# Optimization experiments

Measured on AMD Instinct MI355X. Metric: run time of the kernel, lower is better.

Reference implementation:

```python
import jax, jax.numpy as jnp
import numpy as np
from jax import lax

THRESHOLD = 0.25
DECAY = 0.9
STRIDE = 1
PADDING = 1


def setup_inputs() -> dict:
    key = jax.random.key(0)
    k1, k2 = jax.random.split(key)
    # binary spike train: (B, C_in, H, W, T)
    x = (jax.random.uniform(k1, (8, 16, 64, 64, 32)) < 0.2).astype(jnp.float32)
    # conv weight: (C_out, C_in, k, k), init ~ randn * 0.1 as in the torch module
    weight = jax.random.normal(k2, (32, 16, 3, 3), dtype=jnp.float32) * 0.1
    return {"x": x, "weight": weight}


def _conv(xt, weight):
    # xt: (B, C_in, H, W) -> (B, C_out, H_out, W_out)
    return lax.conv_general_dilated(
        xt, weight,
        window_strides=(STRIDE, STRIDE),
        padding=[(PADDING, PADDING), (PADDING, PADDING)],
        dimension_numbers=("NCHW", "OIHW", "NCHW"),
    )


def reference(x, weight):
    B, Cin, H, W, T = x.shape
    Cout, k = weight.shape[0], weight.shape[2]
    Hout = (H + 2 * PADDING - k) // STRIDE + 1
    Wout = (W + 2 * PADDING - k) // STRIDE + 1

    xt = jnp.moveaxis(x, -1, 0)  # (T, B, Cin, H, W)
    mem0 = jnp.zeros((B, Cout, Hout, Wout), dtype=jnp.float32)

    def step(mem, x_t):
        # accumulate conv activation, then decay (order matches original: += then *=)
        mem = (mem + _conv(x_t, weight)) * DECAY
        spike = (mem >= THRESHOLD).astype(mem.dtype)
        mem = mem * (1.0 - spike)  # reset fired neurons to 0
        return mem, spike

    _, spikes = lax.scan(step, mem0, xt)  # spikes: (T, B, Cout, Hout, Wout)
    return jnp.moveaxis(spikes, 0, -1)    # (B, Cout, Hout, Wout, T)
```

## Files before the change

kernel.cpp:

```cpp
#include <hip/hip_runtime.h>


#define BB   8
#define CIN  16
#define HH   64
#define WW   64
#define TT   32
#define COUT 32
#define HWT  (HH * WW * TT)

__global__ void repack_w(const float* __restrict__ wgt, float* __restrict__ wT) {
    const int e = blockIdx.x * 256 + threadIdx.x;
    if (e < 144 * 32) {
        const int co  = e & 31;
        const int tau = e >> 5;
        const int ci  = tau & 15;
        const int khw = tau >> 4;
        wT[tau * 32 + co] = wgt[co * 144 + ci * 9 + khw];
    }
}

__global__ __launch_bounds__(256)
void snn_main(const float* __restrict__ x, const float* __restrict__ wT,
              float* __restrict__ out) {
    const int tid  = threadIdx.x;
    const int lane = tid & 63;
    const int t    = lane & 31;
    const int wi   = (tid >> 5);
    const int w0   = blockIdx.x * 8;
    const int h    = blockIdx.y;
    const int b    = blockIdx.z;
    const int w    = w0 + wi;

    float acc[COUT];
#pragma unroll
    for (int c = 0; c < COUT; ++c) acc[c] = 0.0f;

#pragma unroll
    for (int kh = 0; kh < 3; ++kh) {
        const int hs = h + kh - 1;
        if ((unsigned)hs >= HH) continue;
#pragma unroll
        for (int kw = 0; kw < 3; ++kw) {
            const int ws    = w + kw - 1;
            const bool ok   = (unsigned)ws < WW;
            const int  wsc  = ok ? ws : 0;
            const float* xp = x + ((b * CIN * HH + hs) * WW + wsc) * TT + t;
#pragma unroll
            for (int ci = 0; ci < CIN; ++ci) {
                float xv = xp[ci * HWT];
                xv = ok ? xv : 0.0f;
                const float* wr = wT + ((kh * 3 + kw) * 16 + ci) * 32;
#pragma unroll
                for (int c = 0; c < COUT; ++c)
                    acc[c] = fmaf(xv, wr[c], acc[c]);
            }
        }
    }

    __shared__ float s_tr[256 * 36];
#pragma unroll
    for (int c = 0; c < COUT; ++c)
        s_tr[(c * 8 + wi) * 36 + t] = acc[c];
    __syncthreads();

    const int co2 = tid >> 3;
    const int wi2 = tid & 7;
    const float* rr = s_tr + (co2 * 8 + wi2) * 36;

    float* op = out + (((b * COUT + co2) * HH + h) * WW + (w0 + wi2)) * TT;
    float mem = 0.0f;
#pragma unroll
    for (int t4 = 0; t4 < TT; t4 += 4) {
        const float4 q = *reinterpret_cast<const float4*>(rr + t4);
        const float cv[4] = {q.x, q.y, q.z, q.w};
        float4 o;
        float* vp = &o.x;
#pragma unroll
        for (int j = 0; j < 4; ++j) {
            mem = (mem + cv[j]) * 0.9f;
            const bool sp = (mem >= 0.25f);
            vp[j] = sp ? 1.0f : 0.0f;
            if (sp) mem = 0.0f;
        }
        *reinterpret_cast<float4*>(op + t4) = o;
    }
}

extern "C" void kernel_launch(void* const* d_in, const int* in_sizes, int n_in,
                              void* d_out, int out_size, void* d_ws, size_t ws_size,
                              hipStream_t stream) {
    const float* x   = (const float*)d_in[0];
    const float* wgt = (const float*)d_in[1];
    float* out = (float*)d_out;
    float* wT  = (float*)d_ws;

    repack_w<<<18, 256, 0, stream>>>(wgt, wT);

    dim3 grid(WW / 8, HH, BB);
    snn_main<<<grid, dim3(256), 0, stream>>>(x, wT, out);
}
```

Measured before the change: 281.2 us.

## Use packed FP32 FMA, halve LDS transpose buffer, raise occupancy bound

Accumulators become 2-wide float vectors so the compiler can emit packed FP32 FMAs (v_pk_fma_f32) and take weights as 64-bit pairs. The shared-memory transpose buffer is halved and the scan runs in two passes over 16 channels each, so LDS per block drops. The launch bound requests 8 blocks per CU. The trade-offs are an extra barrier, half the threads idle during each scan pass, and possible register spills under the tighter bound.

```diff
diff --git a/kernel.cpp b/kernel.cpp
--- a/kernel.cpp
+++ b/kernel.cpp
@@ -8,6 +8,8 @@
 #define TT   32
 #define COUT 32
 #define HWT  (HH * WW * TT)
+
+typedef float f32x2 __attribute__((ext_vector_type(2)));
 
 __global__ void repack_w(const float* __restrict__ wgt, float* __restrict__ wT) {
     const int e = blockIdx.x * 256 + threadIdx.x;
@@ -20,21 +22,20 @@
     }
 }
 
-__global__ __launch_bounds__(256)
+__global__ __launch_bounds__(256, 8)
 void snn_main(const float* __restrict__ x, const float* __restrict__ wT,
               float* __restrict__ out) {
-    const int tid  = threadIdx.x;
-    const int lane = tid & 63;
-    const int t    = lane & 31;
-    const int wi   = (tid >> 5);
-    const int w0   = blockIdx.x * 8;
-    const int h    = blockIdx.y;
-    const int b    = blockIdx.z;
-    const int w    = w0 + wi;
+    const int tid = threadIdx.x;
+    const int t   = tid & 31;
+    const int wi  = tid >> 5;
+    const int w0  = blockIdx.x * 8;
+    const int h   = blockIdx.y;
+    const int b   = blockIdx.z;
+    const int w   = w0 + wi;
 
-    float acc[COUT];
+    f32x2 acc2[16];
 #pragma unroll
-    for (int c = 0; c < COUT; ++c) acc[c] = 0.0f;
+    for (int i = 0; i < 16; ++i) acc2[i] = (f32x2){0.0f, 0.0f};
 
 #pragma unroll
     for (int kh = 0; kh < 3; ++kh) {
@@ -42,48 +43,57 @@
         if ((unsigned)hs >= HH) continue;
 #pragma unroll
         for (int kw = 0; kw < 3; ++kw) {
-            const int ws    = w + kw - 1;
-            const bool ok   = (unsigned)ws < WW;
-            const int  wsc  = ok ? ws : 0;
-            const float* xp = x + ((b * CIN * HH + hs) * WW + wsc) * TT + t;
+            const int ws  = w + kw - 1;
+            const bool ok = (unsigned)ws < WW;
+            const int wsc = ok ? ws : 0;
+            const float* xp  = x + ((b * CIN * HH + hs) * WW + wsc) * TT + t;
+            const f32x2* wr2 = (const f32x2*)(wT + (kh * 3 + kw) * (CIN * 32));
 #pragma unroll
             for (int ci = 0; ci < CIN; ++ci) {
                 float xv = xp[ci * HWT];
                 xv = ok ? xv : 0.0f;
-                const float* wr = wT + ((kh * 3 + kw) * 16 + ci) * 32;
+                const f32x2 xv2 = {xv, xv};
 #pragma unroll
-                for (int c = 0; c < COUT; ++c)
-                    acc[c] = fmaf(xv, wr[c], acc[c]);
+                for (int c2 = 0; c2 < 16; ++c2)
+                    acc2[c2] = __builtin_elementwise_fma(xv2, wr2[ci * 16 + c2],
+                                                         acc2[c2]);
             }
         }
     }
 
-    __shared__ float s_tr[256 * 36];
+    __shared__ float s_tr[128 * 36];
 #pragma unroll
-    for (int c = 0; c < COUT; ++c)
-        s_tr[(c * 8 + wi) * 36 + t] = acc[c];
-    __syncthreads();
-
-    const int co2 = tid >> 3;
-    const int wi2 = tid & 7;
-    const float* rr = s_tr + (co2 * 8 + wi2) * 36;
-
-    float* op = out + (((b * COUT + co2) * HH + h) * WW + (w0 + wi2)) * TT;
-    float mem = 0.0f;
+    for (int p = 0; p < 2; ++p) {
+        if (p) __syncthreads();
 #pragma unroll
-    for (int t4 = 0; t4 < TT; t4 += 4) {
-        const float4 q = *reinterpret_cast<const float4*>(rr + t4);
-        const float cv[4] = {q.x, q.y, q.z, q.w};
-        float4 o;
-        float* vp = &o.x;
+        for (int j = 0; j < 16; ++j) {
+            const int c = 16 * p + j;
+            s_tr[(j * 8 + wi) * 36 + t] = acc2[c >> 1][c & 1];
+        }
+        __syncthreads();
+        if (tid < 128) {
+            const int j2  = tid >> 3;
+            const int wi2 = tid & 7;
+            const int co2 = 16 * p + j2;
+            const float* rr = s_tr + tid * 36;
+            float* op = out + (((b * COUT + co2) * HH + h) * WW + (w0 + wi2)) * TT;
+            float mem = 0.0f;
 #pragma unroll
-        for (int j = 0; j < 4; ++j) {
-            mem = (mem + cv[j]) * 0.9f;
-            const bool sp = (mem >= 0.25f);
-            vp[j] = sp ? 1.0f : 0.0f;
-            if (sp) mem = 0.0f;
+            for (int t4 = 0; t4 < TT; t4 += 4) {
+                const float4 q = *reinterpret_cast<const float4*>(rr + t4);
+                const float cv[4] = {q.x, q.y, q.z, q.w};
+                float4 o;
+                float* vp = &o.x;
+#pragma unroll
+                for (int jj = 0; jj < 4; ++jj) {
+                    mem = (mem + cv[jj]) * 0.9f;
+                    const bool sp = (mem >= 0.25f);
+                    vp[jj] = sp ? 1.0f : 0.0f;
+                    if (sp) mem = 0.0f;
+                }
+                *reinterpret_cast<float4*>(op + t4) = o;
+            }
         }
-        *reinterpret_cast<float4*>(op + t4) = o;
     }
 }
 
```

New measurement: 278.0 us. Within noise of the previous version (-1.1%).
